# Kernel tuning notes

Hardware: AMD Instinct MI355X
Metric: run time of the kernel (lower is better)

The kernel has to match this reference:

```python
import jax, jax.numpy as jnp
import numpy as np

EMBED_DIM = 2048
NUM_HEADS = 32
NUM_SEQS = 8
SEQ_LEN = 1024
TOTAL_TOKENS = NUM_SEQS * SEQ_LEN


def setup_inputs() -> dict:
    key = jax.random.key(0)
    ks = jax.random.split(key, 9)
    E = EMBED_DIM
    std = 0.02
    return {
        "hidden_states": jax.random.normal(ks[0], (TOTAL_TOKENS, E), dtype=jnp.float32),
        "Wq": jax.random.normal(ks[1], (E, E), dtype=jnp.float32) * std,
        "bq": jax.random.normal(ks[2], (E,), dtype=jnp.float32) * std,
        "Wk": jax.random.normal(ks[3], (E, E), dtype=jnp.float32) * std,
        "bk": jax.random.normal(ks[4], (E,), dtype=jnp.float32) * std,
        "Wv": jax.random.normal(ks[5], (E, E), dtype=jnp.float32) * std,
        "bv": jax.random.normal(ks[6], (E,), dtype=jnp.float32) * std,
        "Wo": jax.random.normal(ks[7], (E, E), dtype=jnp.float32) * std,
        "bo": jax.random.normal(ks[8], (E,), dtype=jnp.float32) * std,
        "seq_len": SEQ_LEN,
    }


def reference(hidden_states, Wq, bq, Wk, bk, Wv, bv, Wo, bo, seq_len):
    # OPTAttention (has_cache=False): block-diagonal causal attention over
    # packed ragged sequences; here all NUM_SEQS sequences have length seq_len,
    # so the block-diagonal mask is exactly per-sequence causal attention.
    T, E = hidden_states.shape
    H = NUM_HEADS
    D = E // H
    B = T // seq_len
    scaling = D ** -0.5

    # torch nn.Linear: y = x @ W.T + b
    q = hidden_states @ Wq.T + bq
    k = hidden_states @ Wk.T + bk
    v = hidden_states @ Wv.T + bv

    q = q.reshape(B, seq_len, H, D)
    k = k.reshape(B, seq_len, H, D)
    v = v.reshape(B, seq_len, H, D)

    # [B, H, S, S] attention scores (xformers applies scale to q@k.T)
    scores = jnp.einsum("bqhd,bkhd->bhqk", q, k) * scaling
    causal = jnp.tril(jnp.ones((seq_len, seq_len), dtype=bool))
    scores = jnp.where(causal[None, None, :, :], scores, jnp.finfo(scores.dtype).min)
    probs = jax.nn.softmax(scores, axis=-1)

    attn = jnp.einsum("bhqk,bkhd->bqhd", probs, v)  # [B, S, H, D]
    attn = attn.reshape(T, E)
    return attn @ Wo.T + bo
```

## Files before the change

### kernel.cpp

```cpp
#include <hip/hip_runtime.h>
#include <hip/hip_bf16.h>

typedef __bf16 bf16_t;
typedef __bf16 bf16x8 __attribute__((ext_vector_type(8)));
typedef __bf16 bf16x4 __attribute__((ext_vector_type(4)));
typedef float f32x4 __attribute__((ext_vector_type(4)));
typedef float f32x16 __attribute__((ext_vector_type(16)));
typedef unsigned short u16x8 __attribute__((ext_vector_type(8)));
typedef unsigned int u32x4 __attribute__((ext_vector_type(4)));

#define T_TOK 8192
#define E_DIM 2048
#define NHEAD 32
#define SEQLEN 1024
#define NSEQ 8
#define LDQ 6144

#if __has_builtin(__builtin_amdgcn_exp2f)
#define EXP2F(x) __builtin_amdgcn_exp2f(x)
#else
#define EXP2F(x) exp2f(x)
#endif

static __device__ inline unsigned cvtpk_bf16(float lo, float hi) {
    unsigned r;
    asm("v_cvt_pk_bf16_f32 %0, %1, %2" : "=v"(r) : "v"(lo), "v"(hi));
    return r;
}

static __device__ inline void plswap(unsigned &x, unsigned &y, bool lo_half) {
#if __has_builtin(__builtin_amdgcn_permlane32_swap)
    auto r = __builtin_amdgcn_permlane32_swap(x, y, false, false);
    x = r[0]; y = r[1];
#else
    unsigned xs = __shfl_xor(x, 32), ys = __shfl_xor(y, 32);
    unsigned nx = lo_half ? x : ys;
    unsigned ny = lo_half ? xs : y;
    x = nx; y = ny;
#endif
}

__global__ void cvt_all(const float* __restrict__ hid, const float* __restrict__ Wq,
                        const float* __restrict__ Wk, const float* __restrict__ Wv,
                        const float* __restrict__ Wo, bf16_t* __restrict__ hidB,
                        bf16_t* __restrict__ Wcat, bf16_t* __restrict__ WoB) {
    const int TE4 = (T_TOK * E_DIM) / 4;
    const int EE4 = (E_DIM * E_DIM) / 4;
    const float* src;
    bf16_t* dst;
    int n4, base, nb;
    const int bid = blockIdx.x;
    if (bid < 2048)      { src = hid; dst = hidB;              n4 = TE4; base = 0;    nb = 2048; }
    else if (bid < 2560) { src = Wq;  dst = Wcat;              n4 = EE4; base = 2048; nb = 512; }
    else if (bid < 3072) { src = Wk;  dst = Wcat + 4 * EE4;    n4 = EE4; base = 2560; nb = 512; }
    else if (bid < 3584) { src = Wv;  dst = Wcat + 8 * EE4;    n4 = EE4; base = 3072; nb = 512; }
    else                 { src = Wo;  dst = WoB;               n4 = EE4; base = 3584; nb = 512; }
    const int stride = nb * 256;
    for (int i = (bid - base) * 256 + threadIdx.x; i < n4; i += stride) {
        const float4 v = reinterpret_cast<const float4*>(src)[i];
        bf16x4 o;
        o[0] = (bf16_t)v.x; o[1] = (bf16_t)v.y; o[2] = (bf16_t)v.z; o[3] = (bf16_t)v.w;
        reinterpret_cast<bf16x4*>(dst)[i] = o;
    }
}

template<bool OUT_BF16>
__global__ __launch_bounds__(512, 2)
void gemm256f(const bf16_t* __restrict__ A, const bf16_t* __restrict__ B,
              const float* __restrict__ b0, const float* __restrict__ b1,
              const float* __restrict__ b2, void* __restrict__ Cout,
              int M, int N, float qs, int qlim) {
    constexpr int K = 2048;
    constexpr int NK = K / 32;
    __shared__ alignas(16) unsigned char lds[131072];
    const int tid = threadIdx.x;
    const int wid = tid >> 6, l = tid & 63;
    const int cpx = gridDim.x >> 3;
    const int id = (blockIdx.x & 7) * cpx + (blockIdx.x >> 3);
    const int sb = id >> 5, si = id & 31;
    const int smw = (M >> 8) >> 3;
    const int bm = (sb % smw) * 8 + (si & 7);
    const int bn = (sb / smw) * 4 + (si >> 3);
    const int wrow = (wid >> 2) * 128, wcol = (wid & 3) * 64;
    const int lr = l & 15, lg = l >> 4;

    f32x4 acc[8][4] = {};

    const bf16_t* aBase = A + (size_t)(bm * 256) * K;
    const bf16_t* bBase = B + (size_t)(bn * 256) * K;
    const int sr = l >> 2;
    const int sc = (l & 3) * 16;

    auto stage = [&](int t) {
        unsigned char* base = lds + (t & 3) * 32768;
#pragma unroll
        for (int c = 0; c < 2; ++c) {
            const int chunk = wid * 2 + c;
            const int r = chunk * 16 + sr;
            const int cb = sc ^ (((r >> 1) & 3) << 4);
            __builtin_amdgcn_global_load_lds(
                (const __attribute__((address_space(1))) void*)(aBase + (size_t)r * K + t * 32 + (cb >> 1)),
                (__attribute__((address_space(3))) void*)(base + chunk * 1024), 16, 0, 0);
            __builtin_amdgcn_global_load_lds(
                (const __attribute__((address_space(1))) void*)(bBase + (size_t)r * K + t * 32 + (cb >> 1)),
                (__attribute__((address_space(3))) void*)(base + 16384 + chunk * 1024), 16, 0, 0);
        }
    };

    bf16x8 fa0[8], fb0[4], fa1[8], fb1[4];

    stage(0); stage(1); stage(2);
    asm volatile("s_waitcnt vmcnt(4)" ::: "memory");
    __builtin_amdgcn_s_barrier();
    {
        const unsigned char* Ab = lds;
        const unsigned char* Bb = Ab + 16384;
#pragma unroll
        for (int n = 0; n < 4; ++n) {
            const int r = wcol + n * 16 + lr;
            fb0[n] = *reinterpret_cast<const bf16x8*>(Bb + r * 64 + ((lg * 16) ^ (((r >> 1) & 3) << 4)));
        }
#pragma unroll
        for (int m = 0; m < 8; ++m) {
            const int r = wrow + m * 16 + lr;
            fa0[m] = *reinterpret_cast<const bf16x8*>(Ab + r * 64 + ((lg * 16) ^ (((r >> 1) & 3) << 4)));
        }
    }

    auto step = [&](int t, bf16x8 (&ca)[8], bf16x8 (&cb)[4],
                    bf16x8 (&na)[8], bf16x8 (&nb)[4]) {
        if (t + 3 < NK) stage(t + 3);
        const unsigned char* Nb = lds + ((t + 1) & 3) * 32768;
        const unsigned char* NbB = Nb + 16384;
        __builtin_amdgcn_s_setprio(1);
#pragma unroll
        for (int m = 0; m < 8; ++m) {
            if (m < 4) {
                const int rb = wcol + m * 16 + lr;
                nb[m] = *reinterpret_cast<const bf16x8*>(NbB + rb * 64 + ((lg * 16) ^ (((rb >> 1) & 3) << 4)));
            }
            const int ra = wrow + m * 16 + lr;
            na[m] = *reinterpret_cast<const bf16x8*>(Nb + ra * 64 + ((lg * 16) ^ (((ra >> 1) & 3) << 4)));
#pragma unroll
            for (int n = 0; n < 4; ++n)
                acc[m][n] = __builtin_amdgcn_mfma_f32_16x16x32_bf16(ca[m], cb[n], acc[m][n], 0, 0, 0);
        }
        __builtin_amdgcn_s_setprio(0);
        if (t < NK - 1) {
            if (t + 3 < NK) asm volatile("s_waitcnt vmcnt(4)" ::: "memory");
            else            asm volatile("s_waitcnt vmcnt(0)" ::: "memory");
            __builtin_amdgcn_s_barrier();
        }
    };

#pragma unroll 1
    for (int t = 0; t < NK; t += 2) {
        step(t,     fa0, fb0, fa1, fb1);
        step(t + 1, fa1, fb1, fa0, fb0);
    }

    const int r0 = bm * 256 + wrow + lg * 4;
    const int c0 = bn * 256 + wcol + lr;
#pragma unroll
    for (int n = 0; n < 4; ++n) {
        const int cc = c0 + n * 16;
        const float bias = (cc < 2048) ? b0[cc] : (cc < 4096 ? b1[cc - 2048] : b2[cc - 4096]);
        const float sc2 = (cc < qlim) ? qs : 1.0f;
#pragma unroll
        for (int m = 0; m < 8; ++m)
#pragma unroll
            for (int j = 0; j < 4; ++j) {
                const int rr = r0 + m * 16 + j;
                const float v = (acc[m][n][j] + bias) * sc2;
                if (OUT_BF16) ((bf16_t*)Cout)[(size_t)rr * N + cc] = (bf16_t)v;
                else          ((float*)Cout)[(size_t)rr * N + cc] = v;
            }
    }
}

__global__ __launch_bounds__(512, 2)
void attn_fwd3(const bf16_t* __restrict__ QKV, bf16_t* __restrict__ Og) {
    const int orig = blockIdx.x;
    const int id = (orig & 7) * 64 + (orig >> 3);
    const int grp = id >> 1;
    const int pairIdx = id & 1;
    const int h = grp & 31;
    const int sq = grp >> 5;

    const int tid = threadIdx.x;
    const int w = tid >> 6;
    const int l = tid & 63;
    const int ll = l & 31;
    const int hi = l >> 5;
    const bool lo_half = (hi == 0);

    __shared__ alignas(16) unsigned char lds[65536];

    const bf16_t* Qg = QKV;
    const bf16_t* Kg = QKV + 2048;
    const bf16_t* Vg = QKV + 4096;
    const size_t kvbase = (size_t)(sq * SEQLEN) * LDQ + h * 64;

    bf16x8 vr0, vr1;
    const int vk0 = l * 2;
    const int vd0 = w * 8;

    auto stageK = [&](int kt, int buf) {
#pragma unroll
        for (int c = 0; c < 2; ++c) {
            const int o = (w * 2 + c) * 1024 + l * 16;
            const int r = o >> 7;
            const int swb = (o & 127) ^ ((r & 7) << 4);
            const bf16_t* src = Kg + kvbase + (size_t)(kt * 128 + r) * LDQ + (swb >> 1);
            __builtin_amdgcn_global_load_lds(
                (const __attribute__((address_space(1))) void*)src,
                (__attribute__((address_space(3))) void*)(lds + buf * 16384 + (w * 2 + c) * 1024),
                16, 0, 0);
        }
    };
    auto loadV = [&](int kt) {
        const bf16_t* vp = Vg + kvbase + (size_t)(kt * 128 + vk0) * LDQ + vd0;
        vr0 = *reinterpret_cast<const bf16x8*>(vp);
        vr1 = *reinterpret_cast<const bf16x8*>(vp + LDQ);
    };
    auto writeV = [&](int buf) {
        u16x8 s0 = __builtin_bit_cast(u16x8, vr0);
        u16x8 s1 = __builtin_bit_cast(u16x8, vr1);
        unsigned char* vb = lds + 32768 + buf * 16384;
#pragma unroll
        for (int e = 0; e < 8; ++e) {
            const int d = vd0 + e;
            unsigned off = (unsigned)(d * 256 + vk0 * 2);
            off ^= ((unsigned)((d ^ (d >> 4)) & 15)) << 4;
            *reinterpret_cast<unsigned*>(vb + off) = (unsigned)s0[e] | ((unsigned)s1[e] << 16);
        }
    };

    const unsigned ksw = (unsigned)((l & 7) << 4);
    const unsigned kbase = (unsigned)(ll * 128 + hi * 16);

#pragma unroll 1
    for (int seg = 0; seg < 2; ++seg) {
        const int qt = pairIdx ? (seg ? 2 : 1) : (seg ? 3 : 0);

        const int q_glob = qt * 256 + w * 32 + ll;
        const bf16_t* qp = Qg + (size_t)(sq * SEQLEN + q_glob) * LDQ + h * 64 + hi * 8;
        bf16x8 qf[4];
#pragma unroll
        for (int dc = 0; dc < 4; ++dc)
            qf[dc] = *reinterpret_cast<const bf16x8*>(qp + dc * 16);

        const int nkt = 2 * qt + 2;
        const int q_wave_max = qt * 256 + w * 32 + 31;

        f32x16 oac[2] = {};
        float mrun = -3.0e38f, lsum = 0.f;

        stageK(0, 0);
        loadV(0);
        writeV(0);
        __syncthreads();

        int cur = 0;
        for (int kt = 0; kt < nkt; ++kt) {
            const bool notlast = (kt + 1 < nkt);
            if (notlast) { stageK(kt + 1, cur ^ 1); loadV(kt + 1); }

            if (kt * 128 <= q_wave_max) {
                const unsigned char* Kcur = lds + cur * 16384;
                const unsigned char* Vcur = lds + 32768 + cur * 16384;

                f32x16 st[4];
#pragma unroll
                for (int kh = 0; kh < 4; ++kh) {
                    f32x16 acc = {};
#pragma unroll
                    for (int dc = 0; dc < 4; ++dc) {
                        const unsigned off = (kbase + (unsigned)(kh * 4096 + dc * 32)) ^ ksw;
                        const bf16x8 ka = *reinterpret_cast<const bf16x8*>(Kcur + off);
                        acc = __builtin_amdgcn_mfma_f32_32x32x16_bf16(ka, qf[dc], acc, 0, 0, 0);
                    }
                    st[kh] = acc;
                }

                if (kt >= 2 * qt) {
#pragma unroll
                    for (int kh = 0; kh < 4; ++kh)
#pragma unroll
                        for (int r = 0; r < 16; ++r) {
                            const int kg = kt * 128 + kh * 32 + (r & 3) + 8 * (r >> 2) + 4 * hi;
                            if (kg > q_glob) st[kh][r] = -3.0e38f;
                        }
                }

                float tm = -3.0e38f;
#pragma unroll
                for (int kh = 0; kh < 4; ++kh)
#pragma unroll
                    for (int r = 0; r < 16; ++r) tm = fmaxf(tm, st[kh][r]);
                tm = fmaxf(tm, __shfl_xor(tm, 32));

                if (!__all(tm <= mrun + 8.0f)) {
                    const float mnew = fmaxf(mrun, tm);
                    const float rsc = EXP2F(mrun - mnew);
                    mrun = mnew;
                    lsum *= rsc;
#pragma unroll
                    for (int dh = 0; dh < 2; ++dh)
#pragma unroll
                        for (int r = 0; r < 16; ++r) oac[dh][r] *= rsc;
                }

                float ps = 0.f;
#pragma unroll
                for (int kh = 0; kh < 4; ++kh)
#pragma unroll
                    for (int r = 0; r < 16; ++r) {
                        const float p = EXP2F(st[kh][r] - mrun);
                        st[kh][r] = p;
                        ps += p;
                    }
                ps += __shfl_xor(ps, 32);
                lsum += ps;

                bf16x8 pf[8];
#pragma unroll
                for (int kh = 0; kh < 4; ++kh)
#pragma unroll
                    for (int hc = 0; hc < 2; ++hc) {
                        const int b0i = hc * 8;
                        unsigned a  = cvtpk_bf16(st[kh][b0i + 0], st[kh][b0i + 1]);
                        unsigned b  = cvtpk_bf16(st[kh][b0i + 4], st[kh][b0i + 5]);
                        unsigned a2 = cvtpk_bf16(st[kh][b0i + 2], st[kh][b0i + 3]);
                        unsigned b2 = cvtpk_bf16(st[kh][b0i + 6], st[kh][b0i + 7]);
                        plswap(a, b, lo_half);
                        plswap(a2, b2, lo_half);
                        u32x4 words = { a, a2, b, b2 };
                        pf[kh * 2 + hc] = __builtin_bit_cast(bf16x8, words);
                    }

#pragma unroll
                for (int dh = 0; dh < 2; ++dh) {
                    const int d = dh * 32 + ll;
                    const unsigned vsw = ((unsigned)((d ^ (d >> 4)) & 15)) << 4;
                    const unsigned vbb = (unsigned)(d * 256 + hi * 16);
#pragma unroll
                    for (int kc = 0; kc < 8; ++kc) {
                        const unsigned off = (vbb + (unsigned)(kc * 32)) ^ vsw;
                        const bf16x8 vfr = *reinterpret_cast<const bf16x8*>(Vcur + off);
                        oac[dh] = __builtin_amdgcn_mfma_f32_32x32x16_bf16(vfr, pf[kc], oac[dh], 0, 0, 0);
                    }
                }
            }

            if (notlast) writeV(cur ^ 1);
            __syncthreads();
            cur ^= 1;
        }

        const float inv = 1.0f / lsum;
        bf16_t* op = Og + (size_t)(sq * SEQLEN + q_glob) * E_DIM + h * 64;
#pragma unroll
        for (int dh = 0; dh < 2; ++dh)
#pragma unroll
            for (int rq = 0; rq < 4; ++rq) {
                const int d0 = dh * 32 + 8 * rq + 4 * hi;
                bf16x4 ov;
#pragma unroll
                for (int j = 0; j < 4; ++j)
                    ov[j] = (bf16_t)(oac[dh][rq * 4 + j] * inv);
                *reinterpret_cast<bf16x4*>(op + d0) = ov;
            }
    }
}

extern "C" void kernel_launch(void* const* d_in, const int* in_sizes, int n_in,
                              void* d_out, int out_size, void* d_ws, size_t ws_size,
                              hipStream_t stream) {
    const float* hid = (const float*)d_in[0];
    const float* Wq  = (const float*)d_in[1];
    const float* bq  = (const float*)d_in[2];
    const float* Wk  = (const float*)d_in[3];
    const float* bk  = (const float*)d_in[4];
    const float* Wv  = (const float*)d_in[5];
    const float* bv  = (const float*)d_in[6];
    const float* Wo  = (const float*)d_in[7];
    const float* bo  = (const float*)d_in[8];
    float* out = (float*)d_out;

    const size_t TE = (size_t)T_TOK * E_DIM;
    const size_t EE = (size_t)E_DIM * E_DIM;

    bf16_t* ws   = (bf16_t*)d_ws;
    bf16_t* hidB = ws;
    bf16_t* qkvB = ws + TE;
    bf16_t* Wcat = qkvB + 3 * TE;
    bf16_t* WoB  = Wcat + 3 * EE;

    cvt_all<<<4096, 256, 0, stream>>>(hid, Wq, Wk, Wv, Wo, hidB, Wcat, WoB);

    const float QSCALE = 0.125f * 1.4426950408889634f;

    gemm256f<true><<<dim3((T_TOK / 256) * (LDQ / 256)), 512, 0, stream>>>(
        hidB, Wcat, bq, bk, bv, qkvB, T_TOK, LDQ, QSCALE, 2048);

    attn_fwd3<<<dim3(512), 512, 0, stream>>>(qkvB, hidB);

    gemm256f<false><<<dim3((T_TOK / 256) * (E_DIM / 256)), 512, 0, stream>>>(
        hidB, WoB, bo, bo, bo, out, T_TOK, E_DIM, 1.0f, 0);
}
```

Baseline: 385.6 us.

## Replace 256x256 GEMM with 256x128 tile, 4-wave blocks and triple-buffered LDS

Both projection GEMMs now use 256-thread blocks, each computing a 256x128 output tile. The LDS ring shrinks from four 32KB slots to three 24KB slots with prefetch distance two. The register double-buffering of fragments is dropped: each iteration loads its fragments from LDS and then issues the MFMAs. The intent is a smaller LDS footprint and more blocks for better occupancy and wave balance. The cost is lower arithmetic intensity per block and less overlap between LDS reads and MFMA work.

Result: slower. 399.4 us (+3.6%).

```diff
diff --git a/kernel.cpp b/kernel.cpp
--- a/kernel.cpp
+++ b/kernel.cpp
@@ -65,14 +65,15 @@
 }
 
 template<bool OUT_BF16>
-__global__ __launch_bounds__(512, 2)
-void gemm256f(const bf16_t* __restrict__ A, const bf16_t* __restrict__ B,
-              const float* __restrict__ b0, const float* __restrict__ b1,
-              const float* __restrict__ b2, void* __restrict__ Cout,
-              int M, int N, float qs, int qlim) {
+__global__ __launch_bounds__(256, 2)
+void gemm2b(const bf16_t* __restrict__ A, const bf16_t* __restrict__ B,
+            const float* __restrict__ b0, const float* __restrict__ b1,
+            const float* __restrict__ b2, void* __restrict__ Cout,
+            int M, int N, float qs, int qlim) {
     constexpr int K = 2048;
     constexpr int NK = K / 32;
-    __shared__ alignas(16) unsigned char lds[131072];
+    constexpr int SLOT = 24576;
+    __shared__ alignas(16) unsigned char lds[3 * SLOT];
     const int tid = threadIdx.x;
     const int wid = tid >> 6, l = tid & 63;
     const int cpx = gridDim.x >> 3;
@@ -81,86 +82,74 @@
     const int smw = (M >> 8) >> 3;
     const int bm = (sb % smw) * 8 + (si & 7);
     const int bn = (sb / smw) * 4 + (si >> 3);
-    const int wrow = (wid >> 2) * 128, wcol = (wid & 3) * 64;
+    const int wrow = (wid >> 1) * 128, wcol = (wid & 1) * 64;
     const int lr = l & 15, lg = l >> 4;
 
     f32x4 acc[8][4] = {};
 
     const bf16_t* aBase = A + (size_t)(bm * 256) * K;
-    const bf16_t* bBase = B + (size_t)(bn * 256) * K;
+    const bf16_t* bBase = B + (size_t)(bn * 128) * K;
     const int sr = l >> 2;
     const int sc = (l & 3) * 16;
 
-    auto stage = [&](int t) {
-        unsigned char* base = lds + (t & 3) * 32768;
-#pragma unroll
-        for (int c = 0; c < 2; ++c) {
-            const int chunk = wid * 2 + c;
+    auto stage = [&](int t, int slot) {
+        unsigned char* base = lds + slot * SLOT;
+#pragma unroll
+        for (int i = 0; i < 4; ++i) {
+            const int chunk = wid + 4 * i;
             const int r = chunk * 16 + sr;
             const int cb = sc ^ (((r >> 1) & 3) << 4);
             __builtin_amdgcn_global_load_lds(
                 (const __attribute__((address_space(1))) void*)(aBase + (size_t)r * K + t * 32 + (cb >> 1)),
                 (__attribute__((address_space(3))) void*)(base + chunk * 1024), 16, 0, 0);
+        }
+#pragma unroll
+        for (int i = 0; i < 2; ++i) {
+            const int chunk = wid + 4 * i;
+            const int r = chunk * 16 + sr;
+            const int cb = sc ^ (((r >> 1) & 3) << 4);
             __builtin_amdgcn_global_load_lds(
                 (const __attribute__((address_space(1))) void*)(bBase + (size_t)r * K + t * 32 + (cb >> 1)),
                 (__attribute__((address_space(3))) void*)(base + 16384 + chunk * 1024), 16, 0, 0);
         }
     };
 
-    bf16x8 fa0[8], fb0[4], fa1[8], fb1[4];
-
-    stage(0); stage(1); stage(2);
-    asm volatile("s_waitcnt vmcnt(4)" ::: "memory");
+    stage(0, 0); stage(1, 1);
+    asm volatile("s_waitcnt vmcnt(6)" ::: "memory");
     __builtin_amdgcn_s_barrier();
-    {
-        const unsigned char* Ab = lds;
+
+#pragma unroll 1
+    for (int t = 0; t < NK; ++t) {
+        const int sl = t % 3;
+        if (t + 2 < NK) stage(t + 2, (t + 2) % 3);
+        const unsigned char* Ab = lds + sl * SLOT;
         const unsigned char* Bb = Ab + 16384;
+        bf16x8 bfv[4], af[8];
 #pragma unroll
         for (int n = 0; n < 4; ++n) {
             const int r = wcol + n * 16 + lr;
-            fb0[n] = *reinterpret_cast<const bf16x8*>(Bb + r * 64 + ((lg * 16) ^ (((r >> 1) & 3) << 4)));
+            bfv[n] = *reinterpret_cast<const bf16x8*>(Bb + r * 64 + ((lg * 16) ^ (((r >> 1) & 3) << 4)));
         }
 #pragma unroll
         for (int m = 0; m < 8; ++m) {
             const int r = wrow + m * 16 + lr;
-            fa0[m] = *reinterpret_cast<const bf16x8*>(Ab + r * 64 + ((lg * 16) ^ (((r >> 1) & 3) << 4)));
-        }
+            af[m] = *reinterpret_cast<const bf16x8*>(Ab + r * 64 + ((lg * 16) ^ (((r >> 1) & 3) << 4)));
+        }
+        __builtin_amdgcn_s_setprio(1);
+#pragma unroll
+        for (int m = 0; m < 8; ++m)
+#pragma unroll
+            for (int n = 0; n < 4; ++n)
+                acc[m][n] = __builtin_amdgcn_mfma_f32_16x16x32_bf16(af[m], bfv[n], acc[m][n], 0, 0, 0);
+        __builtin_amdgcn_s_setprio(0);
+        if (t == NK - 1) break;
+        if (t + 2 < NK) asm volatile("s_waitcnt vmcnt(6)" ::: "memory");
+        else            asm volatile("s_waitcnt vmcnt(0)" ::: "memory");
+        __builtin_amdgcn_s_barrier();
     }
 
-    auto step = [&](int t, bf16x8 (&ca)[8], bf16x8 (&cb)[4],
-                    bf16x8 (&na)[8], bf16x8 (&nb)[4]) {
-        if (t + 3 < NK) stage(t + 3);
-        const unsigned char* Nb = lds + ((t + 1) & 3) * 32768;
-        const unsigned char* NbB = Nb + 16384;
-        __builtin_amdgcn_s_setprio(1);
-#pragma unroll
-        for (int m = 0; m < 8; ++m) {
-            if (m < 4) {
-                const int rb = wcol + m * 16 + lr;
-                nb[m] = *reinterpret_cast<const bf16x8*>(NbB + rb * 64 + ((lg * 16) ^ (((rb >> 1) & 3) << 4)));
-            }
-            const int ra = wrow + m * 16 + lr;
-            na[m] = *reinterpret_cast<const bf16x8*>(Nb + ra * 64 + ((lg * 16) ^ (((ra >> 1) & 3) << 4)));
-#pragma unroll
-            for (int n = 0; n < 4; ++n)
-                acc[m][n] = __builtin_amdgcn_mfma_f32_16x16x32_bf16(ca[m], cb[n], acc[m][n], 0, 0, 0);
-        }
-        __builtin_amdgcn_s_setprio(0);
-        if (t < NK - 1) {
-            if (t + 3 < NK) asm volatile("s_waitcnt vmcnt(4)" ::: "memory");
-            else            asm volatile("s_waitcnt vmcnt(0)" ::: "memory");
-            __builtin_amdgcn_s_barrier();
-        }
-    };
-
-#pragma unroll 1
-    for (int t = 0; t < NK; t += 2) {
-        step(t,     fa0, fb0, fa1, fb1);
-        step(t + 1, fa1, fb1, fa0, fb0);
-    }
-
     const int r0 = bm * 256 + wrow + lg * 4;
-    const int c0 = bn * 256 + wcol + lr;
+    const int c0 = bn * 128 + wcol + lr;
 #pragma unroll
     for (int n = 0; n < 4; ++n) {
         const int cc = c0 + n * 16;
@@ -401,11 +390,11 @@
 
     const float QSCALE = 0.125f * 1.4426950408889634f;
 
-    gemm256f<true><<<dim3((T_TOK / 256) * (LDQ / 256)), 512, 0, stream>>>(
+    gemm2b<true><<<dim3((T_TOK / 256) * (LDQ / 128)), 256, 0, stream>>>(
         hidB, Wcat, bq, bk, bv, qkvB, T_TOK, LDQ, QSCALE, 2048);
 
     attn_fwd3<<<dim3(512), 512, 0, stream>>>(qkvB, hidB);
 
-    gemm256f<false><<<dim3((T_TOK / 256) * (E_DIM / 256)), 512, 0, stream>>>(
+    gemm2b<false><<<dim3((T_TOK / 256) * (E_DIM / 128)), 256, 0, stream>>>(
         hidB, WoB, bo, bo, bo, out, T_TOK, E_DIM, 1.0f, 0);
 }
```
